# Kernel tuning notes

Hardware: AMD Instinct MI355X
Metric: run time of the kernel (lower is better)

The kernel has to match this reference:

```python
import jax, jax.numpy as jnp
import numpy as np

# Dims forced/chosen per module code: n_embd=256 hardcoded via torch.split(x, 256, dim=2)
B, S, E, H, D, L, V, NI = 4, 2048, 256, 8, 32, 2, 50257, 1024
EPS = 1e-5
MASK_VALUE = -10000.0
INIT_STD = 0.02


def _layernorm(x, g, b):
    mu = jnp.mean(x, axis=-1, keepdims=True)
    var = jnp.var(x, axis=-1, keepdims=True)
    return (x - mu) * jax.lax.rsqrt(var + EPS) * g + b


def setup_inputs() -> dict:
    key = jax.random.key(0)
    ks = jax.random.split(key, 8)
    s = INIT_STD
    return {
        "input_ids": jax.random.randint(ks[0], (B, S), 0, V),
        "wte": jax.random.normal(ks[1], (V, E), dtype=jnp.float32) * s,
        "wpe": jax.random.normal(ks[2], (S, E), dtype=jnp.float32) * s,
        # per-layer params stacked on leading L axis (for lax.scan)
        "ln1_g": jnp.ones((L, E)), "ln1_b": jnp.zeros((L, E)),
        "qkv_w": jax.random.normal(ks[3], (L, E, 3 * E), dtype=jnp.float32) * s,
        "qkv_b": jnp.zeros((L, 3 * E)),
        "proj_w": jax.random.normal(ks[4], (L, E, E), dtype=jnp.float32) * s,
        "proj_b": jnp.zeros((L, E)),
        "ln2_g": jnp.ones((L, E)), "ln2_b": jnp.zeros((L, E)),
        "fc1_w": jax.random.normal(ks[5], (L, E, NI), dtype=jnp.float32) * s,
        "fc1_b": jnp.zeros((L, NI)),
        "fc2_w": jax.random.normal(ks[6], (L, NI, E), dtype=jnp.float32) * s,
        "fc2_b": jnp.zeros((L, E)),
        "lnf_g": jnp.ones((E,)), "lnf_b": jnp.zeros((E,)),
    }


def _forward(input_ids, wte, wpe, ln1_g, ln1_b, qkv_w, qkv_b, proj_w, proj_b,
             ln2_g, ln2_b, fc1_w, fc1_b, fc2_w, fc2_b, lnf_g, lnf_b):
    h = wte[input_ids] + wpe[jnp.arange(S)]  # [B,S,E]; embd dropout p=0 -> identity
    causal = jnp.tril(jnp.ones((S, S), dtype=bool))  # built each call, as in source
    scale = jnp.asarray(1.0 / np.sqrt(D), dtype=h.dtype)

    def block(h, p):
        g1, b1, Wqkv, bqkv, Wp, bp, g2, b2, W1, b1m, W2, b2m = p
        x = _layernorm(h, g1, b1)
        qkv = x @ Wqkv + bqkv                     # [B,S,3E]
        q, k, v = jnp.split(qkv, 3, axis=-1)      # torch.split(x, 256, dim=2)
        heads = lambda t: t.reshape(B, S, H, D).transpose(0, 2, 1, 3)  # [B,H,S,D]
        q, k, v = heads(q), heads(k), heads(v)
        scores = jnp.einsum('bhqd,bhkd->bhqk', q, k) * scale
        scores = jnp.where(causal, scores, MASK_VALUE)  # masked_fill with -10000.0
        probs = jax.nn.softmax(scores, axis=-1)         # attn dropout p=0 -> identity
        out = jnp.einsum('bhqk,bhkd->bhqd', probs, v)
        out = out.transpose(0, 2, 1, 3).reshape(B, S, E)
        h = h + (out @ Wp + bp)                   # resid dropout p=0 -> identity
        x2 = _layernorm(h, g2, b2)
        m = jax.nn.gelu(x2 @ W1 + b1m, approximate=True) @ W2 + b2m  # gelu_new (tanh)
        return h + m, None

    h, _ = jax.lax.scan(block, h, (ln1_g, ln1_b, qkv_w, qkv_b, proj_w, proj_b,
                                   ln2_g, ln2_b, fc1_w, fc1_b, fc2_w, fc2_b))
    return _layernorm(h, lnf_g, lnf_b)


def reference(input_ids, wte, wpe, ln1_g, ln1_b, qkv_w, qkv_b, proj_w, proj_b,
              ln2_g, ln2_b, fc1_w, fc1_b, fc2_w, fc2_b, lnf_g, lnf_b):
    return _forward(input_ids, wte, wpe, ln1_g, ln1_b, qkv_w, qkv_b, proj_w,
                    proj_b, ln2_g, ln2_b, fc1_w, fc1_b, fc2_w, fc2_b, lnf_g, lnf_b)
```

## Files before the change

kernel.cpp:

```cpp
#include <hip/hip_runtime.h>
#include <hip/hip_bf16.h>
#include <math.h>

#define BB 4
#define SS 2048
#define EE 256
#define HH 8
#define DD 32
#define LL 2
#define NI 1024
#define NROWS (BB*SS)
#define NRL   (BB*HH*SS)

typedef float f32x4 __attribute__((ext_vector_type(4)));
typedef short s16x8 __attribute__((ext_vector_type(8)));
typedef __bf16 bf16x8 __attribute__((ext_vector_type(8)));
typedef unsigned short ushort_t;

#define QSCALE 0.2550352699458294f

__device__ __forceinline__ unsigned short f2bf(float f) {
    return __builtin_bit_cast(unsigned short, (__bf16)f);
}
__device__ __forceinline__ float bf2f(unsigned short s) {
    return __uint_as_float((unsigned)s << 16);
}
__device__ __forceinline__ f32x4 mfma16x16x32(s16x8 a, s16x8 b, f32x4 c) {
    return __builtin_amdgcn_mfma_f32_16x16x32_bf16(
        __builtin_bit_cast(bf16x8, a), __builtin_bit_cast(bf16x8, b), c, 0, 0, 0);
}

__global__ __launch_bounds__(256) void embed_ln_kernel(
    const int* __restrict__ ids, const float* __restrict__ wte,
    const float* __restrict__ wpe, const float* __restrict__ g,
    const float* __restrict__ b, float* __restrict__ h, ushort_t* __restrict__ x)
{
    int row  = blockIdx.x * 4 + (threadIdx.x >> 6);
    int s    = row & (SS - 1);
    int lane = threadIdx.x & 63;
    int id   = ids[row];
    float4 a = *(const float4*)(wte + (size_t)id * EE + lane * 4);
    float4 p = *(const float4*)(wpe + (size_t)s  * EE + lane * 4);
    float4 v = { a.x + p.x, a.y + p.y, a.z + p.z, a.w + p.w };
    *(float4*)(h + (size_t)row * EE + lane * 4) = v;
    float sm  = v.x + v.y + v.z + v.w;
    float ss2 = v.x*v.x + v.y*v.y + v.z*v.z + v.w*v.w;
    #pragma unroll
    for (int off = 32; off; off >>= 1) {
        sm  += __shfl_xor(sm,  off);
        ss2 += __shfl_xor(ss2, off);
    }
    float mu  = sm * (1.f / EE);
    float var = ss2 * (1.f / EE) - mu * mu;
    float rs  = rsqrtf(var + 1e-5f);
    float4 gv = *(const float4*)(g + lane * 4);
    float4 bv = *(const float4*)(b + lane * 4);
    ushort4 w = { f2bf((v.x - mu) * rs * gv.x + bv.x),
                  f2bf((v.y - mu) * rs * gv.y + bv.y),
                  f2bf((v.z - mu) * rs * gv.z + bv.z),
                  f2bf((v.w - mu) * rs * gv.w + bv.w) };
    *(ushort4*)(x + (size_t)row * EE + lane * 4) = w;
}

template<bool OUTBF>
__global__ __launch_bounds__(256) void ln_kernel(
    const float* __restrict__ in, const float* __restrict__ g,
    const float* __restrict__ b, void* __restrict__ out)
{
    int row  = blockIdx.x * 4 + (threadIdx.x >> 6);
    int lane = threadIdx.x & 63;
    float4 v = *(const float4*)(in + (size_t)row * EE + lane * 4);
    float s  = v.x + v.y + v.z + v.w;
    float ss = v.x*v.x + v.y*v.y + v.z*v.z + v.w*v.w;
    #pragma unroll
    for (int off = 32; off; off >>= 1) {
        s  += __shfl_xor(s,  off);
        ss += __shfl_xor(ss, off);
    }
    float mu  = s * (1.f / EE);
    float var = ss * (1.f / EE) - mu * mu;
    float rs  = rsqrtf(var + 1e-5f);
    float4 gv = *(const float4*)(g + lane * 4);
    float4 bv = *(const float4*)(b + lane * 4);
    float4 o;
    o.x = (v.x - mu) * rs * gv.x + bv.x;
    o.y = (v.y - mu) * rs * gv.y + bv.y;
    o.z = (v.z - mu) * rs * gv.z + bv.z;
    o.w = (v.w - mu) * rs * gv.w + bv.w;
    if (OUTBF) {
        ushort4 w = { f2bf(o.x), f2bf(o.y), f2bf(o.z), f2bf(o.w) };
        *(ushort4*)((ushort_t*)out + (size_t)row * EE + lane * 4) = w;
    } else {
        *(float4*)((float*)out + (size_t)row * EE + lane * 4) = o;
    }
}

__global__ __launch_bounds__(256) void wconv_all(
    const float* __restrict__ qkv_w, const float* __restrict__ proj_w,
    const float* __restrict__ fc1_w, const float* __restrict__ fc2_w,
    ushort_t* __restrict__ wq_t, ushort_t* __restrict__ wp_t,
    ushort_t* __restrict__ w1_t, ushort_t* __restrict__ w2_t)
{
    __shared__ float t_[32][33];
    int l = blockIdx.y, t = blockIdx.x;
    const float* W; ushort_t* Wt; int K, N, n0, k0;
    if (t < 192)      { W = qkv_w  + (size_t)l*EE*3*EE; Wt = wq_t + (size_t)l*3*EE*EE;
                        K = EE; N = 3*EE; int u = t;       n0 = (u % 24) * 32; k0 = (u / 24) * 32; }
    else if (t < 256) { W = proj_w + (size_t)l*EE*EE;   Wt = wp_t + (size_t)l*EE*EE;
                        K = EE; N = EE;   int u = t - 192; n0 = (u % 8)  * 32; k0 = (u / 8)  * 32; }
    else if (t < 512) { W = fc1_w  + (size_t)l*EE*NI;   Wt = w1_t + (size_t)l*EE*NI;
                        K = EE; N = NI;   int u = t - 256; n0 = (u % 32) * 32; k0 = (u / 32) * 32; }
    else              { W = fc2_w  + (size_t)l*NI*EE;   Wt = w2_t + (size_t)l*NI*EE;
                        K = NI; N = EE;   int u = t - 512; n0 = (u % 8)  * 32; k0 = (u / 8)  * 32; }
    int tx = threadIdx.x & 31, ty = threadIdx.x >> 5;
    #pragma unroll
    for (int i = 0; i < 4; ++i) {
        int k = ty + i * 8;
        t_[k][tx] = W[(size_t)(k0 + k) * N + n0 + tx];
    }
    __syncthreads();
    #pragma unroll
    for (int i = 0; i < 4; ++i) {
        int n = ty + i * 8;
        Wt[(size_t)(n0 + n) * K + k0 + tx] = f2bf(t_[tx][n]);
    }
}

template<int MI, bool OUT_BF, bool GELU_ACT, bool RES, bool QSC>
__global__ __launch_bounds__(256) void gemm_bf(
    const ushort_t* __restrict__ A, const ushort_t* __restrict__ Bt,
    const float* __restrict__ bias, const float* __restrict__ res,
    void* __restrict__ C, int M, int N, int K)
{
    __shared__ __align__(16) ushort_t As[MI*64][40];
    __shared__ __align__(16) ushort_t Bs[64][40];
    int tid = threadIdx.x;
    int wid = tid >> 6, lane = tid & 63;
    int h = lane >> 4, c = lane & 15;
    int bx = blockIdx.x, by = blockIdx.y;

    f32x4 acc[MI][4] = {};

    int arow = tid >> 2, ac = tid & 3;
    const ushort_t* Ap = A  + (size_t)(by * (MI*64) + arow) * K + ac * 8;
    const ushort_t* Bp = Bt + (size_t)(bx * 64     + arow) * K + ac * 8;

    s16x8 av[MI], bv;
    #pragma unroll
    for (int i = 0; i < MI; ++i)
        av[i] = *(const s16x8*)(Ap + (size_t)i * 64 * K);
    bv = *(const s16x8*)(Bp);

    for (int k0 = 0; k0 < K; k0 += 32) {
        __syncthreads();
        #pragma unroll
        for (int i = 0; i < MI; ++i)
            *(s16x8*)&As[i * 64 + arow][ac * 8] = av[i];
        *(s16x8*)&Bs[arow][ac * 8] = bv;
        if (k0 + 32 < K) {
            #pragma unroll
            for (int i = 0; i < MI; ++i)
                av[i] = *(const s16x8*)(Ap + (size_t)i * 64 * K + k0 + 32);
            bv = *(const s16x8*)(Bp + k0 + 32);
        }
        asm volatile("s_waitcnt lgkmcnt(0)" ::: "memory");
        __builtin_amdgcn_s_barrier();
        asm volatile("" ::: "memory");

        s16x8 af[MI], bfr[4];
        #pragma unroll
        for (int i = 0; i < MI; ++i)
            af[i] = *(const s16x8*)&As[wid * (MI*16) + i * 16 + c][h * 8];
        #pragma unroll
        for (int j = 0; j < 4; ++j)
            bfr[j] = *(const s16x8*)&Bs[j * 16 + c][h * 8];
        #pragma unroll
        for (int i = 0; i < MI; ++i)
            #pragma unroll
            for (int j = 0; j < 4; ++j)
                acc[i][j] = mfma16x16x32(af[i], bfr[j], acc[i][j]);
    }

    float bj[4];
    #pragma unroll
    for (int j = 0; j < 4; ++j) bj[j] = bias[bx * 64 + j * 16 + c];
    #pragma unroll
    for (int i = 0; i < MI; ++i) {
        #pragma unroll
        for (int r = 0; r < 4; ++r) {
            int row = by * (MI*64) + wid * (MI*16) + i * 16 + h * 4 + r;
            #pragma unroll
            for (int j = 0; j < 4; ++j) {
                int col = bx * 64 + j * 16 + c;
                float v = acc[i][j][r] + bj[j];
                if (QSC && col < EE) v *= QSCALE;
                if (RES) v += res[(size_t)row * N + col];
                if (GELU_ACT) {
                    float t = v;
                    v = 0.5f * t * (1.f + tanhf(0.7978845608028654f *
                                                (t + 0.044715f * t * t * t)));
                }
                if (OUT_BF) ((ushort_t*)C)[(size_t)row * N + col] = f2bf(v);
                else        ((float*)C)[(size_t)row * N + col]    = v;
            }
        }
    }
}

#define QB 64
#define KSTR 40
#define VSTR 88
#define PSTR 72
#define PTILES 8
__global__ __launch_bounds__(256) void attn_kernel(
    const ushort_t* __restrict__ qkv, ushort_t* __restrict__ o_part,
    float* __restrict__ l_part, ushort_t* __restrict__ attno)
{
    __shared__ __align__(16) ushort_t Ks[QB][KSTR];
    __shared__ __align__(16) ushort_t Vt[DD][VSTR];
    __shared__ __align__(16) ushort_t Ps[4][16][PSTR];

    int tid  = threadIdx.x;
    int p    = 79 - blockIdx.x;
    int qt, ks;
    if (p < 8)       { qt = p;                 ks = 0; }
    else if (p < 24) { qt = 8  + ((p-8)  >> 1); ks = (p-8)  & 1; }
    else if (p < 48) { qt = 16 + (p-24) / 3;    ks = (p-24) % 3; }
    else             { qt = 24 + ((p-48) >> 2); ks = (p-48) & 3; }
    int hh   = blockIdx.y, b = blockIdx.z;
    int wid  = tid >> 6, lane = tid & 63;
    int h    = lane >> 4, c = lane & 15;

    int qfrow = qt * QB + wid * 16 + c;
    s16x8 qfrag = *(const s16x8*)(qkv + ((size_t)(b * SS + qfrow)) * (3*EE)
                                  + hh * DD + h * 8);

    s16x8 onesf = { (short)0x3F80, (short)0x3F80, (short)0x3F80, (short)0x3F80,
                    (short)0x3F80, (short)0x3F80, (short)0x3F80, (short)0x3F80 };

    f32x4 o0 = {0.f,0.f,0.f,0.f}, o1 = {0.f,0.f,0.f,0.f}, o2 = {0.f,0.f,0.f,0.f};

    int srow = tid >> 2, scq = tid & 3;
    int t0 = ks * PTILES;
    int t1 = min(t0 + PTILES, qt + 1);

    s16x8 kreg, vreg;
    {
        const ushort_t* kb = qkv + ((size_t)(b * SS + t0 * QB)) * (3*EE) + hh * DD + EE;
        kreg = *(const s16x8*)(kb + (size_t)srow * (3*EE) + scq * 8);
        vreg = *(const s16x8*)(kb + EE + (size_t)srow * (3*EE) + scq * 8);
    }

    for (int kt = t0; kt < t1; ++kt) {
        int k0 = kt * QB;

        __syncthreads();

        *(s16x8*)&Ks[srow][scq * 8] = kreg;
        {
            int d0 = scq * 8;
            int colw = srow ^ (scq << 4);
            #pragma unroll
            for (int j = 0; j < 8; ++j) Vt[d0 + j][colw] = (ushort_t)vreg[j];
        }
        if (kt + 1 < t1) {
            const ushort_t* kb2 = qkv + ((size_t)(b * SS + (kt+1) * QB)) * (3*EE)
                                  + hh * DD + EE;
            kreg = *(const s16x8*)(kb2 + (size_t)srow * (3*EE) + scq * 8);
            vreg = *(const s16x8*)(kb2 + EE + (size_t)srow * (3*EE) + scq * 8);
        }

        asm volatile("s_waitcnt lgkmcnt(0)" ::: "memory");
        __builtin_amdgcn_s_barrier();
        asm volatile("" ::: "memory");

        __builtin_amdgcn_s_setprio(1);

        f32x4 sg[4];
        #pragma unroll
        for (int g = 0; g < 4; ++g) {
            s16x8 kf = *(const s16x8*)&Ks[g * 16 + c][h * 8];
            f32x4 z = {0.f,0.f,0.f,0.f};
            sg[g] = mfma16x16x32(kf, qfrag, z);
        }

        bool diag = (kt == qt);
        int klim = qfrow - k0;

        #pragma unroll
        for (int g = 0; g < 4; ++g) {
            ushort4 pk;
            #pragma unroll
            for (int r = 0; r < 4; ++r) {
                float x = sg[g][r];
                if (diag && (g * 16 + h * 4 + r > klim)) x = -INFINITY;
                ((ushort_t*)&pk)[r] = f2bf(exp2f(x));
            }
            *(ushort4*)&Ps[wid][c][g * 16 + h * 4] = pk;
        }

        #pragma unroll
        for (int kc = 0; kc < 2; ++kc) {
            int kbase = kc * 32 + h * 8;
            s16x8 pf = *(const s16x8*)&Ps[wid][c][kbase];
            s16x8 v0 = *(const s16x8*)&Vt[c]     [kbase ^ ((c >> 3) << 4)];
            s16x8 v1 = *(const s16x8*)&Vt[16 + c][kbase ^ (((16 + c) >> 3) << 4)];
            o0 = mfma16x16x32(pf, v0, o0);
            o1 = mfma16x16x32(pf, v1, o1);
            o2 = mfma16x16x32(pf, onesf, o2);
        }

        __builtin_amdgcn_s_setprio(0);
    }

    if (qt < PTILES) {
        #pragma unroll
        for (int r = 0; r < 4; ++r) {
            int qrow = qt * QB + wid * 16 + h * 4 + r;
            float inv = 1.f / o2[r];
            ushort_t* ap = attno + ((size_t)(b * SS + qrow)) * EE + hh * DD;
            ap[c]      = f2bf(o0[r] * inv);
            ap[16 + c] = f2bf(o1[r] * inv);
        }
    } else {
        size_t rbase = (size_t)(b * HH + hh) * SS;
        #pragma unroll
        for (int r = 0; r < 4; ++r) {
            int qrow = qt * QB + wid * 16 + h * 4 + r;
            size_t rl = rbase + qrow;
            ushort_t* op = o_part + ((size_t)ks * NRL + rl) * DD;
            op[c]      = f2bf(o0[r]);
            op[16 + c] = f2bf(o1[r]);
            if (c == 0) l_part[(size_t)ks * NRL + rl] = o2[r];
        }
    }
}

__global__ __launch_bounds__(256) void attn_merge(
    const ushort_t* __restrict__ o_part, const float* __restrict__ l_part,
    ushort_t* __restrict__ attno)
{
    int g = blockIdx.x * 256 + threadIdx.x;
    int rl = g >> 3;
    int d0 = (g & 7) * 4;
    int srow = rl & (SS - 1);
    int qt = srow >> 6;
    if (qt < PTILES) return;
    int np = (qt >> 3) + 1;

    float acc0 = 0.f, acc1 = 0.f, acc2 = 0.f, acc3 = 0.f, L = 0.f;
    #pragma unroll
    for (int i = 0; i < 4; ++i) {
        if (i < np) {
            L += l_part[(size_t)i * NRL + rl];
            ushort4 ov = *(const ushort4*)(o_part + ((size_t)i * NRL + rl) * DD + d0);
            acc0 += bf2f(ov.x); acc1 += bf2f(ov.y);
            acc2 += bf2f(ov.z); acc3 += bf2f(ov.w);
        }
    }
    float inv = 1.f / L;
    int b  = rl >> 14;
    int hh = (rl >> 11) & 7;
    ushort4 w4 = { f2bf(acc0*inv), f2bf(acc1*inv), f2bf(acc2*inv), f2bf(acc3*inv) };
    *(ushort4*)(attno + ((size_t)(b * SS + srow)) * EE + hh * DD + d0) = w4;
}

extern "C" void kernel_launch(void* const* d_in, const int* in_sizes, int n_in,
                              void* d_out, int out_size, void* d_ws, size_t ws_size,
                              hipStream_t stream)
{
    const int*   ids    = (const int*)  d_in[0];
    const float* wte    = (const float*)d_in[1];
    const float* wpe    = (const float*)d_in[2];
    const float* ln1_g  = (const float*)d_in[3];
    const float* ln1_b  = (const float*)d_in[4];
    const float* qkv_w  = (const float*)d_in[5];
    const float* qkv_b  = (const float*)d_in[6];
    const float* proj_w = (const float*)d_in[7];
    const float* proj_b = (const float*)d_in[8];
    const float* ln2_g  = (const float*)d_in[9];
    const float* ln2_b  = (const float*)d_in[10];
    const float* fc1_w  = (const float*)d_in[11];
    const float* fc1_b  = (const float*)d_in[12];
    const float* fc2_w  = (const float*)d_in[13];
    const float* fc2_b  = (const float*)d_in[14];
    const float* lnf_g  = (const float*)d_in[15];
    const float* lnf_b  = (const float*)d_in[16];

    float*    h        = (float*)d_ws;
    ushort_t* x_bf     = (ushort_t*)(h + (size_t)NROWS*EE);
    ushort_t* qkv_bf   = x_bf   + (size_t)NROWS*EE;
    ushort_t* attno_bf = qkv_bf + (size_t)NROWS*3*EE;
    ushort_t* m1_bf    = attno_bf + (size_t)NROWS*EE;
    ushort_t* wq_t     = m1_bf  + (size_t)NROWS*NI;
    ushort_t* wp_t     = wq_t   + (size_t)2*3*EE*EE;
    ushort_t* w1_t     = wp_t   + (size_t)2*EE*EE;
    ushort_t* w2_t     = w1_t   + (size_t)2*EE*NI;

    ushort_t* o_part   = m1_bf;
    float*    l_part   = (float*)x_bf;

    wconv_all<<<dim3(768, LL), 256, 0, stream>>>(
        qkv_w, proj_w, fc1_w, fc2_w, wq_t, wp_t, w1_t, w2_t);

    embed_ln_kernel<<<NROWS/4, 256, 0, stream>>>(ids, wte, wpe, ln1_g, ln1_b, h, x_bf);

    for (int l = 0; l < LL; ++l) {
        if (l > 0)
            ln_kernel<true><<<NROWS/4, 256, 0, stream>>>(h, ln1_g + l*EE, ln1_b + l*EE, x_bf);
        gemm_bf<2,true,false,false,true><<<dim3(3*EE/64, NROWS/128), 256, 0, stream>>>(
            x_bf, wq_t + (size_t)l*3*EE*EE, qkv_b + (size_t)l*3*EE, nullptr,
            qkv_bf, NROWS, 3*EE, EE);
        attn_kernel<<<dim3(80, HH, BB), 256, 0, stream>>>(qkv_bf, o_part, l_part, attno_bf);
        attn_merge<<<NRL*8/256, 256, 0, stream>>>(o_part, l_part, attno_bf);
        gemm_bf<1,false,false,true,false><<<dim3(EE/64, NROWS/64), 256, 0, stream>>>(
            attno_bf, wp_t + (size_t)l*EE*EE, proj_b + (size_t)l*EE, h,
            h, NROWS, EE, EE);
        ln_kernel<true><<<NROWS/4, 256, 0, stream>>>(h, ln2_g + l*EE, ln2_b + l*EE, x_bf);
        gemm_bf<2,true,true,false,false><<<dim3(NI/64, NROWS/128), 256, 0, stream>>>(
            x_bf, w1_t + (size_t)l*EE*NI, fc1_b + (size_t)l*NI, nullptr,
            m1_bf, NROWS, NI, EE);
        gemm_bf<1,false,false,true,false><<<dim3(EE/64, NROWS/64), 256, 0, stream>>>(
            m1_bf, w2_t + (size_t)l*NI*EE, fc2_b + (size_t)l*EE, h,
            h, NROWS, EE, NI);
    }

    ln_kernel<false><<<NROWS/4, 256, 0, stream>>>(h, lnf_g, lnf_b, (float*)d_out);
}
```

Measured before the change: 204.1 us.

## Remap GEMM workgroups across XCDs and deepen global prefetch to two stages

Workgroup IDs are remapped so that consecutive flat IDs, which the hardware spreads round-robin across the 8 XCDs, are handled as contiguous tiles on each XCD. The goal is better L2 reuse of A and B tiles. The K loop now covers 64 per iteration with two register prefetch buffers, so global loads are issued two k-steps ahead to hide memory latency. The cost is more registers and an extra barrier per half-step, and the remap assumes the workgroup count is divisible by 8.

Result: faster. 195.4 us (-4.2%).

```diff
diff --git a/kernel.cpp b/kernel.cpp
--- a/kernel.cpp
+++ b/kernel.cpp
@@ -137,7 +137,12 @@
     int tid = threadIdx.x;
     int wid = tid >> 6, lane = tid & 63;
     int h = lane >> 4, c = lane & 15;
-    int bx = blockIdx.x, by = blockIdx.y;
+
+    int nbx = gridDim.x;
+    int nwg = nbx * gridDim.y;
+    int flat = blockIdx.y * nbx + blockIdx.x;
+    int v = (flat & 7) * (nwg >> 3) + (flat >> 3);
+    int bx = v % nbx, by = v / nbx;
 
     f32x4 acc[MI][4] = {};
 
@@ -145,40 +150,75 @@
     const ushort_t* Ap = A  + (size_t)(by * (MI*64) + arow) * K + ac * 8;
     const ushort_t* Bp = Bt + (size_t)(bx * 64     + arow) * K + ac * 8;
 
-    s16x8 av[MI], bv;
-    #pragma unroll
-    for (int i = 0; i < MI; ++i)
-        av[i] = *(const s16x8*)(Ap + (size_t)i * 64 * K);
-    bv = *(const s16x8*)(Bp);
-
-    for (int k0 = 0; k0 < K; k0 += 32) {
-        __syncthreads();
-        #pragma unroll
-        for (int i = 0; i < MI; ++i)
-            *(s16x8*)&As[i * 64 + arow][ac * 8] = av[i];
-        *(s16x8*)&Bs[arow][ac * 8] = bv;
-        if (k0 + 32 < K) {
-            #pragma unroll
-            for (int i = 0; i < MI; ++i)
-                av[i] = *(const s16x8*)(Ap + (size_t)i * 64 * K + k0 + 32);
-            bv = *(const s16x8*)(Bp + k0 + 32);
-        }
+    s16x8 a0[MI], a1[MI], b0, b1;
+    #pragma unroll
+    for (int i = 0; i < MI; ++i) a0[i] = *(const s16x8*)(Ap + (size_t)i * 64 * K);
+    b0 = *(const s16x8*)(Bp);
+    #pragma unroll
+    for (int i = 0; i < MI; ++i) a1[i] = *(const s16x8*)(Ap + (size_t)i * 64 * K + 32);
+    b1 = *(const s16x8*)(Bp + 32);
+
+    for (int k0 = 0; k0 < K; k0 += 64) {
         asm volatile("s_waitcnt lgkmcnt(0)" ::: "memory");
         __builtin_amdgcn_s_barrier();
         asm volatile("" ::: "memory");
-
-        s16x8 af[MI], bfr[4];
         #pragma unroll
         for (int i = 0; i < MI; ++i)
-            af[i] = *(const s16x8*)&As[wid * (MI*16) + i * 16 + c][h * 8];
-        #pragma unroll
-        for (int j = 0; j < 4; ++j)
-            bfr[j] = *(const s16x8*)&Bs[j * 16 + c][h * 8];
+            *(s16x8*)&As[i * 64 + arow][ac * 8] = a0[i];
+        *(s16x8*)&Bs[arow][ac * 8] = b0;
+        if (k0 + 64 < K) {
+            #pragma unroll
+            for (int i = 0; i < MI; ++i)
+                a0[i] = *(const s16x8*)(Ap + (size_t)i * 64 * K + k0 + 64);
+            b0 = *(const s16x8*)(Bp + k0 + 64);
+        }
+        asm volatile("s_waitcnt lgkmcnt(0)" ::: "memory");
+        __builtin_amdgcn_s_barrier();
+        asm volatile("" ::: "memory");
+        {
+            s16x8 af[MI], bfr[4];
+            #pragma unroll
+            for (int i = 0; i < MI; ++i)
+                af[i] = *(const s16x8*)&As[wid * (MI*16) + i * 16 + c][h * 8];
+            #pragma unroll
+            for (int j = 0; j < 4; ++j)
+                bfr[j] = *(const s16x8*)&Bs[j * 16 + c][h * 8];
+            #pragma unroll
+            for (int i = 0; i < MI; ++i)
+                #pragma unroll
+                for (int j = 0; j < 4; ++j)
+                    acc[i][j] = mfma16x16x32(af[i], bfr[j], acc[i][j]);
+        }
+        asm volatile("s_waitcnt lgkmcnt(0)" ::: "memory");
+        __builtin_amdgcn_s_barrier();
+        asm volatile("" ::: "memory");
         #pragma unroll
         for (int i = 0; i < MI; ++i)
+            *(s16x8*)&As[i * 64 + arow][ac * 8] = a1[i];
+        *(s16x8*)&Bs[arow][ac * 8] = b1;
+        if (k0 + 96 < K) {
+            #pragma unroll
+            for (int i = 0; i < MI; ++i)
+                a1[i] = *(const s16x8*)(Ap + (size_t)i * 64 * K + k0 + 96);
+            b1 = *(const s16x8*)(Bp + k0 + 96);
+        }
+        asm volatile("s_waitcnt lgkmcnt(0)" ::: "memory");
+        __builtin_amdgcn_s_barrier();
+        asm volatile("" ::: "memory");
+        {
+            s16x8 af[MI], bfr[4];
+            #pragma unroll
+            for (int i = 0; i < MI; ++i)
+                af[i] = *(const s16x8*)&As[wid * (MI*16) + i * 16 + c][h * 8];
             #pragma unroll
             for (int j = 0; j < 4; ++j)
-                acc[i][j] = mfma16x16x32(af[i], bfr[j], acc[i][j]);
+                bfr[j] = *(const s16x8*)&Bs[j * 16 + c][h * 8];
+            #pragma unroll
+            for (int i = 0; i < MI; ++i)
+                #pragma unroll
+                for (int j = 0; j < 4; ++j)
+                    acc[i][j] = mfma16x16x32(af[i], bfr[j], acc[i][j]);
+        }
     }
 
     float bj[4];
@@ -192,16 +232,16 @@
             #pragma unroll
             for (int j = 0; j < 4; ++j) {
                 int col = bx * 64 + j * 16 + c;
-                float v = acc[i][j][r] + bj[j];
-                if (QSC && col < EE) v *= QSCALE;
-                if (RES) v += res[(size_t)row * N + col];
+                float v2 = acc[i][j][r] + bj[j];
+                if (QSC && col < EE) v2 *= QSCALE;
+                if (RES) v2 += res[(size_t)row * N + col];
                 if (GELU_ACT) {
-                    float t = v;
-                    v = 0.5f * t * (1.f + tanhf(0.7978845608028654f *
-                                                (t + 0.044715f * t * t * t)));
+                    float t = v2;
+                    v2 = 0.5f * t * (1.f + tanhf(0.7978845608028654f *
+                                                 (t + 0.044715f * t * t * t)));
                 }
-                if (OUT_BF) ((ushort_t*)C)[(size_t)row * N + col] = f2bf(v);
-                else        ((float*)C)[(size_t)row * N + col]    = v;
+                if (OUT_BF) ((ushort_t*)C)[(size_t)row * N + col] = f2bf(v2);
+                else        ((float*)C)[(size_t)row * N + col]    = v2;
             }
         }
     }
```
